# Kernel tuning notes

Hardware: AMD Instinct MI355X
Metric: run time of the kernel (lower is better)

## Reference

```python
import jax, jax.numpy as jnp
import numpy as np
from jax import lax

ROUTINGS = 3  # num_routing iterations


def _squash(v):
    # v: [..., num_atoms]
    norm = jnp.linalg.norm(v, axis=-1, keepdims=True)
    norm_sq = norm * norm
    return v / norm * (norm_sq / (1.0 + norm_sq))


def setup_inputs() -> dict:
    key = jax.random.key(0)
    k1, k2 = jax.random.split(key)
    B, H, Wd, Ci, Ai = 16, 32, 32, 8, 32
    k, Co, Ao = 5, 16, 16
    x = jax.random.normal(k1, (B, H, Wd, Ci, Ai), dtype=jnp.float32)
    # he_normal init for conv kernel [k, k, Ai, Co*Ao]
    fan_in = k * k * Ai
    W = jax.random.normal(k2, (k, k, Ai, Co * Ao), dtype=jnp.float32) * np.sqrt(2.0 / fan_in).astype(np.float32)
    b = jnp.full((1, 1, Co, Ao), 0.1, dtype=jnp.float32)  # constant(0.1) init
    return {"x": x, "W": W, "b": b}


def reference(x, W, b):
    B, H, Wd, Ci, Ai = x.shape
    k = W.shape[0]
    Co_Ao = W.shape[3]
    Co, Ao = b.shape[2], b.shape[3]
    # fold input capsules into the batch, conv over atoms
    xr = jnp.transpose(x, (0, 3, 1, 2, 4)).reshape(B * Ci, H, Wd, Ai)
    conv = lax.conv_general_dilated(
        xr, W, window_strides=(1, 1), padding="SAME",
        dimension_numbers=("NHWC", "HWIO", "NHWC"))  # [B*Ci, H, W, Co*Ao]
    Ho, Wo = conv.shape[1], conv.shape[2]
    votes = conv.reshape(B, Ci, Ho, Wo, Co, Ao)
    # biases broadcast over spatial dims: [1,1,Co,Ao] -> [Ho,Wo,Co,Ao]
    biases = jnp.broadcast_to(b, (Ho, Wo, Co, Ao))
    # dynamic routing (softmax variant): logits init to 0
    logits = jnp.zeros((B, Ci, Ho, Wo, Co), dtype=votes.dtype)
    activation = None
    for _ in range(ROUTINGS):
        route = jax.nn.softmax(logits, axis=-1)           # [B,Ci,Ho,Wo,Co]
        preact = jnp.sum(route[..., None] * votes, axis=1) + biases  # [B,Ho,Wo,Co,Ao]
        activation = _squash(preact)
        # agreement: sum over atoms of votes * activation
        logits = logits + jnp.sum(votes * activation[:, None], axis=-1)
    return activation
```

## Files before the change

### kernel.cpp

```cpp
#include <hip/hip_runtime.h>
#include <hip/hip_fp16.h>
#include <math.h>


typedef _Float16 f16;
typedef __attribute__((ext_vector_type(2))) _Float16 f16x2;
typedef __attribute__((ext_vector_type(8))) _Float16 f16x8;
typedef __attribute__((ext_vector_type(4))) float f32x4;

#define STRIDE_CI 1944
#define XB_OFF 0
#define WT_OFF 9437184

#define VIDX(p, cp, ao, co) ((((((p)*4 + (cp))*16 + (ao))*18) + (co)) + ((p) & 1))

static __device__ __forceinline__ float2 up16(unsigned int u) {
    union { unsigned int u; f16 h[2]; } c; c.u = u;
    return make_float2((float)c.h[0], (float)c.h[1]);
}

static __device__ __forceinline__ float fdot2u(unsigned int a, unsigned int b, float c) {
#if __has_builtin(__builtin_amdgcn_fdot2)
    union { unsigned int u; f16x2 h; } ua, ub;
    ua.u = a; ub.u = b;
    return __builtin_amdgcn_fdot2(ua.h, ub.h, c, false);
#else
    const float2 fa = up16(a), fb = up16(b);
    return c + fa.x * fb.x + fa.y * fb.y;
#endif
}

__global__ void prep(const float* __restrict__ x, const float* __restrict__ W,
                     f16* __restrict__ xb, f16* __restrict__ Wt) {
    __shared__ f16 lw[32 * 260];
    const int tid = threadIdx.x;
    const int bid = blockIdx.x;
    if (bid < 4608) {
        const int e4 = (bid * 256 + tid) * 4;
        const int c = e4 & 255;
        const int pix = e4 >> 8;
        const int wp = pix % 36;
        const int t = pix / 36;
        const int h = t & 31;
        const int b = t >> 5;
        const int w = wp - 2;
        f16 o[4] = {(f16)0.f, (f16)0.f, (f16)0.f, (f16)0.f};
        if ((unsigned)w < 32u) {
            const float4 v = *(const float4*)&x[(((b * 32 + h) * 32 + w) * 256) + c];
            o[0] = (f16)v.x; o[1] = (f16)v.y; o[2] = (f16)v.z; o[3] = (f16)v.w;
        }
        *(unsigned long long*)&xb[e4] = *(unsigned long long*)o;
    } else {
        const int k5 = bid - 4608;
        for (int rep = 0; rep < 32; ++rep) {
            const int idx = rep * 256 + tid;
            const int ai = idx >> 8, cc = idx & 255;
            lw[ai * 260 + cc] = (f16)W[(k5 * 32 + ai) * 256 + cc];
        }
        __syncthreads();
        for (int rep = 0; rep < 32; ++rep) {
            const int o = rep * 256 + tid;
            const int cc = o >> 5, ai = o & 31;
            Wt[k5 * 8192 + o] = lw[ai * 260 + cc];
        }
    }
}

__global__ __launch_bounds__(256, 3)
void caps_v6(const f16* __restrict__ xb, const f16* __restrict__ Wt,
             const float* __restrict__ bptr, float* __restrict__ out) {
    __shared__ __align__(16) unsigned char smraw[36864];
    f16* patch = (f16*)smraw;
    unsigned int* vl = (unsigned int*)smraw;
    __shared__ __align__(16) unsigned int route_l[8 * 16 * 4];
    __shared__ float logit_l[8 * 8 * 17];
    __shared__ float act_l[8 * 16 * 17];
    __shared__ float bias_l[256];

    const int tid = threadIdx.x;
    const int lane = tid & 63;
    const int wv = tid >> 6;
    const int bid = blockIdx.x;
    const int w0 = (bid & 3) * 8;
    const int h = (bid >> 2) & 31;
    const int b = bid >> 7;

    bias_l[tid] = bptr[tid];

    for (int e = tid; e < 1920; e += 256) {
        const int pos = e >> 5;
        const int ci = (e >> 2) & 7;
        const int s = e & 3;
        const int dh = pos / 12, dw = pos - dh * 12;
        const int gh = h + dh - 2;
        f16x8 v = {};
        if ((unsigned)gh < 32u)
            v = *(const f16x8*)&xb[(((b * 32 + gh) * 36) + (w0 + dw)) * 256 + ci * 32 + s * 8];
        *(f16x8*)&patch[ci * STRIDE_CI + pos * 32 + s * 8] = v;
    }
    __syncthreads();

    const int g = lane >> 4;
    const int q = lane & 15;
    const f16* aptr = patch + (lane & 7) * STRIDE_CI + ((lane >> 3) & 1) * 32 + g * 8;
    const f16* bbase = Wt + (wv * 64 + q) * 32 + g * 8;

    f32x4 acc[4][4];
#pragma unroll
    for (int rb = 0; rb < 4; ++rb)
#pragma unroll
        for (int ct = 0; ct < 4; ++ct) acc[rb][ct] = (f32x4)0.f;

    f16x8 Bc[4], Bn[4];
#pragma unroll
    for (int ct = 0; ct < 4; ++ct) {
        Bc[ct] = *(const f16x8*)(bbase + ct * 512);
        Bn[ct] = *(const f16x8*)(bbase + 8192 + ct * 512);
    }

    int k5 = 0;
#pragma unroll
    for (int kh = 0; kh < 5; ++kh) {
#pragma unroll
        for (int kw = 0; kw < 5; ++kw) {
            f16x8 Bf[4];
            if (k5 < 23) {
                const f16* bf = bbase + (k5 + 2) * 8192;
#pragma unroll
                for (int ct = 0; ct < 4; ++ct)
                    Bf[ct] = *(const f16x8*)(bf + ct * 512);
            }
            const f16* ap = aptr + (kh * 12 + kw) * 32;
            f16x8 A[4];
#pragma unroll
            for (int rb = 0; rb < 4; ++rb)
                A[rb] = *(const f16x8*)(ap + rb * 64);
#pragma unroll
            for (int rb = 0; rb < 4; ++rb)
#pragma unroll
                for (int ct = 0; ct < 4; ++ct)
                    acc[rb][ct] = __builtin_amdgcn_mfma_f32_16x16x32_f16(
                        A[rb], Bc[ct], acc[rb][ct], 0, 0, 0);
#pragma unroll
            for (int ct = 0; ct < 4; ++ct) { Bc[ct] = Bn[ct]; Bn[ct] = Bf[ct]; }
            ++k5;
        }
    }
    __syncthreads();

#pragma unroll
    for (int rb = 0; rb < 4; ++rb) {
        const int p = rb * 2 + (g >> 1);
        const int cpb = (g & 1) * 2;
#pragma unroll
        for (int ct = 0; ct < 4; ++ct) {
            const int co = wv * 4 + ct;
            union { f16 h[2]; unsigned int u; } c0, c1;
            c0.h[0] = (f16)acc[rb][ct].x; c0.h[1] = (f16)acc[rb][ct].y;
            c1.h[0] = (f16)acc[rb][ct].z; c1.h[1] = (f16)acc[rb][ct].w;
            vl[VIDX(p, cpb, q, co)] = c0.u;
            vl[VIDX(p, cpb + 1, q, co)] = c1.u;
        }
    }
    __syncthreads();

    const int rp = tid >> 5;
    const int coh = (tid >> 4) & 1;
    const int ao = tid & 15;
    const int pa = tid >> 5, cpa = (tid >> 3) & 3, co8 = tid & 7;
    const int swz = (pa & 1) * 4 + cpa;

    for (int it = 0; it < 3; ++it) {
        if (it > 0) {
            for (int i = tid; i < 1024; i += 256) {
                const int pp = i >> 7, ci = (i >> 4) & 7, co = i & 15;
                float lg = logit_l[(pp * 8 + ci) * 17 + co];
                float mx = lg;
#pragma unroll
                for (int m = 1; m < 16; m <<= 1) mx = fmaxf(mx, __shfl_xor(mx, m));
                float e = __expf(lg - mx);
                float s = e;
#pragma unroll
                for (int m = 1; m < 16; m <<= 1) s += __shfl_xor(s, m);
                const float r = e * __builtin_amdgcn_rcpf(s);
                const float rother = __shfl_xor(r, 16);
                if (((tid >> 4) & 1) == 0) {
                    union { f16 h[2]; unsigned int u; } pk;
                    pk.h[0] = (f16)r; pk.h[1] = (f16)rother;
                    route_l[(pp * 16 + co) * 4 + (ci >> 1)] = pk.u;
                }
            }
            __syncthreads();
        }

        float actv[8];
#pragma unroll
        for (int c8 = 0; c8 < 8; ++c8) {
            const int co = coh * 8 + c8;
            float pr = bias_l[co * 16 + ao];
            uint4 r4;
            if (it == 0) {
                r4.x = r4.y = r4.z = r4.w = 0x2C002C00u;
            } else {
                r4 = *(const uint4*)&route_l[(rp * 16 + co) * 4];
            }
            pr = fdot2u(vl[VIDX(rp, 0, ao, co)], r4.x, pr);
            pr = fdot2u(vl[VIDX(rp, 1, ao, co)], r4.y, pr);
            pr = fdot2u(vl[VIDX(rp, 2, ao, co)], r4.z, pr);
            pr = fdot2u(vl[VIDX(rp, 3, ao, co)], r4.w, pr);
            float sq = pr * pr;
#pragma unroll
            for (int m = 1; m < 16; m <<= 1) sq += __shfl_xor(sq, m);
            const float nrm = __builtin_amdgcn_sqrtf(sq);
            actv[c8] = pr * nrm * __builtin_amdgcn_rcpf(1.f + sq);
        }
#pragma unroll
        for (int c8 = 0; c8 < 8; ++c8)
            act_l[(rp * 16 + coh * 8 + c8) * 17 + ao] = actv[c8];
        __syncthreads();

        if (it < 2) {
            float d00 = 0.f, d01 = 0.f, d10 = 0.f, d11 = 0.f;
#pragma unroll
            for (int a0 = 0; a0 < 16; ++a0) {
                const int a = a0 ^ swz;
                const unsigned int wA = vl[VIDX(pa, cpa, a, co8)];
                const unsigned int wB = vl[VIDX(pa, cpa, a, co8 + 8)];
                const float aA = act_l[(pa * 16 + co8) * 17 + a];
                const float aB = act_l[(pa * 16 + co8 + 8) * 17 + a];
                const float2 fA = up16(wA), fB = up16(wB);
                d00 += fA.x * aA; d01 += fA.y * aA;
                d10 += fB.x * aB; d11 += fB.y * aB;
            }
            float* l0 = &logit_l[(pa * 8 + cpa * 2) * 17 + co8];
            if (it == 0) { l0[0] = d00; l0[17] = d01; l0[8] = d10; l0[25] = d11; }
            else         { l0[0] += d00; l0[17] += d01; l0[8] += d10; l0[25] += d11; }
            __syncthreads();
        }
    }

    const size_t base = ((size_t)((b * 32 + h) * 32 + w0)) * 256;
    for (int i = tid; i < 2048; i += 256) {
        const int pp = i >> 8, co = (i >> 4) & 15, aoo = i & 15;
        out[base + i] = act_l[(pp * 16 + co) * 17 + aoo];
    }
}

extern "C" void kernel_launch(void* const* d_in, const int* in_sizes, int n_in,
                              void* d_out, int out_size, void* d_ws, size_t ws_size,
                              hipStream_t stream) {
    const float* x  = (const float*)d_in[0];
    const float* W  = (const float*)d_in[1];
    const float* bb = (const float*)d_in[2];
    float* out = (float*)d_out;
    f16* xb = (f16*)((char*)d_ws + XB_OFF);
    f16* Wt = (f16*)((char*)d_ws + WT_OFF);

    hipLaunchKernelGGL(prep, dim3(4608 + 25), dim3(256), 0, stream, x, W, xb, Wt);
    hipLaunchKernelGGL(caps_v6, dim3(2048), dim3(256), 0, stream, xb, Wt, bb, out);
}
```

Measured before the change: 156.3 us.

## Prefetch A fragments and remap routing threads to drop act_l round-trips

```diff
diff --git a/kernel.cpp b/kernel.cpp
--- a/kernel.cpp
+++ b/kernel.cpp
@@ -67,14 +67,13 @@
 }
 
 __global__ __launch_bounds__(256, 3)
-void caps_v6(const f16* __restrict__ xb, const f16* __restrict__ Wt,
+void caps_v7(const f16* __restrict__ xb, const f16* __restrict__ Wt,
              const float* __restrict__ bptr, float* __restrict__ out) {
     __shared__ __align__(16) unsigned char smraw[36864];
     f16* patch = (f16*)smraw;
     unsigned int* vl = (unsigned int*)smraw;
-    __shared__ __align__(16) unsigned int route_l[8 * 16 * 4];
+    __shared__ __align__(16) uint4 route_l[8 * 16];
     __shared__ float logit_l[8 * 8 * 17];
-    __shared__ float act_l[8 * 16 * 17];
     __shared__ float bias_l[256];
 
     const int tid = threadIdx.x;
@@ -112,17 +111,28 @@
         for (int ct = 0; ct < 4; ++ct) acc[rb][ct] = (f32x4)0.f;
 
     f16x8 Bc[4], Bn[4];
+    f16x8 Ac[4], An[4];
 #pragma unroll
     for (int ct = 0; ct < 4; ++ct) {
         Bc[ct] = *(const f16x8*)(bbase + ct * 512);
         Bn[ct] = *(const f16x8*)(bbase + 8192 + ct * 512);
     }
+#pragma unroll
+    for (int rb = 0; rb < 4; ++rb)
+        Ac[rb] = *(const f16x8*)(aptr + rb * 64);
 
     int k5 = 0;
 #pragma unroll
     for (int kh = 0; kh < 5; ++kh) {
 #pragma unroll
         for (int kw = 0; kw < 5; ++kw) {
+            if (k5 < 24) {
+                const int n = k5 + 1;
+                const f16* apn = aptr + ((n / 5) * 12 + (n % 5)) * 32;
+#pragma unroll
+                for (int rb = 0; rb < 4; ++rb)
+                    An[rb] = *(const f16x8*)(apn + rb * 64);
+            }
             f16x8 Bf[4];
             if (k5 < 23) {
                 const f16* bf = bbase + (k5 + 2) * 8192;
@@ -130,17 +140,14 @@
                 for (int ct = 0; ct < 4; ++ct)
                     Bf[ct] = *(const f16x8*)(bf + ct * 512);
             }
-            const f16* ap = aptr + (kh * 12 + kw) * 32;
-            f16x8 A[4];
-#pragma unroll
-            for (int rb = 0; rb < 4; ++rb)
-                A[rb] = *(const f16x8*)(ap + rb * 64);
 #pragma unroll
             for (int rb = 0; rb < 4; ++rb)
 #pragma unroll
                 for (int ct = 0; ct < 4; ++ct)
                     acc[rb][ct] = __builtin_amdgcn_mfma_f32_16x16x32_f16(
-                        A[rb], Bc[ct], acc[rb][ct], 0, 0, 0);
+                        Ac[rb], Bc[ct], acc[rb][ct], 0, 0, 0);
+#pragma unroll
+            for (int rb = 0; rb < 4; ++rb) Ac[rb] = An[rb];
 #pragma unroll
             for (int ct = 0; ct < 4; ++ct) { Bc[ct] = Bn[ct]; Bn[ct] = Bf[ct]; }
             ++k5;
@@ -164,11 +171,10 @@
     }
     __syncthreads();
 
-    const int rp = tid >> 5;
-    const int coh = (tid >> 4) & 1;
-    const int ao = tid & 15;
-    const int pa = tid >> 5, cpa = (tid >> 3) & 3, co8 = tid & 7;
-    const int swz = (pa & 1) * 4 + cpa;
+    const int rp  = tid >> 5;
+    const int rco = (tid >> 1) & 15;
+    const int aoh = tid & 1;
+    unsigned int* route_d = (unsigned int*)route_l;
 
     for (int it = 0; it < 3; ++it) {
         if (it > 0) {
@@ -187,62 +193,68 @@
                 if (((tid >> 4) & 1) == 0) {
                     union { f16 h[2]; unsigned int u; } pk;
                     pk.h[0] = (f16)r; pk.h[1] = (f16)rother;
-                    route_l[(pp * 16 + co) * 4 + (ci >> 1)] = pk.u;
+                    route_d[(pp * 16 + co) * 4 + (ci >> 1)] = pk.u;
                 }
             }
             __syncthreads();
         }
 
+        uint4 r4;
+        if (it == 0) {
+            r4.x = r4.y = r4.z = r4.w = 0x2C002C00u;
+        } else {
+            r4 = route_l[rp * 16 + rco];
+        }
+        float pr[8];
+#pragma unroll
+        for (int a8 = 0; a8 < 8; ++a8) {
+            const int ao = aoh * 8 + a8;
+            float v = bias_l[rco * 16 + ao];
+            v = fdot2u(vl[VIDX(rp, 0, ao, rco)], r4.x, v);
+            v = fdot2u(vl[VIDX(rp, 1, ao, rco)], r4.y, v);
+            v = fdot2u(vl[VIDX(rp, 2, ao, rco)], r4.z, v);
+            v = fdot2u(vl[VIDX(rp, 3, ao, rco)], r4.w, v);
+            pr[a8] = v;
+        }
+        float sq = 0.f;
+#pragma unroll
+        for (int a8 = 0; a8 < 8; ++a8) sq += pr[a8] * pr[a8];
+        sq += __shfl_xor(sq, 1);
+        const float scale = __builtin_amdgcn_sqrtf(sq) * __builtin_amdgcn_rcpf(1.f + sq);
         float actv[8];
 #pragma unroll
-        for (int c8 = 0; c8 < 8; ++c8) {
-            const int co = coh * 8 + c8;
-            float pr = bias_l[co * 16 + ao];
-            uint4 r4;
-            if (it == 0) {
-                r4.x = r4.y = r4.z = r4.w = 0x2C002C00u;
-            } else {
-                r4 = *(const uint4*)&route_l[(rp * 16 + co) * 4];
-            }
-            pr = fdot2u(vl[VIDX(rp, 0, ao, co)], r4.x, pr);
-            pr = fdot2u(vl[VIDX(rp, 1, ao, co)], r4.y, pr);
-            pr = fdot2u(vl[VIDX(rp, 2, ao, co)], r4.z, pr);
-            pr = fdot2u(vl[VIDX(rp, 3, ao, co)], r4.w, pr);
-            float sq = pr * pr;
-#pragma unroll
-            for (int m = 1; m < 16; m <<= 1) sq += __shfl_xor(sq, m);
-            const float nrm = __builtin_amdgcn_sqrtf(sq);
-            actv[c8] = pr * nrm * __builtin_amdgcn_rcpf(1.f + sq);
-        }
-#pragma unroll
-        for (int c8 = 0; c8 < 8; ++c8)
-            act_l[(rp * 16 + coh * 8 + c8) * 17 + ao] = actv[c8];
-        __syncthreads();
+        for (int a8 = 0; a8 < 8; ++a8) actv[a8] = pr[a8] * scale;
 
         if (it < 2) {
-            float d00 = 0.f, d01 = 0.f, d10 = 0.f, d11 = 0.f;
-#pragma unroll
-            for (int a0 = 0; a0 < 16; ++a0) {
-                const int a = a0 ^ swz;
-                const unsigned int wA = vl[VIDX(pa, cpa, a, co8)];
-                const unsigned int wB = vl[VIDX(pa, cpa, a, co8 + 8)];
-                const float aA = act_l[(pa * 16 + co8) * 17 + a];
-                const float aB = act_l[(pa * 16 + co8 + 8) * 17 + a];
-                const float2 fA = up16(wA), fB = up16(wB);
-                d00 += fA.x * aA; d01 += fA.y * aA;
-                d10 += fB.x * aB; d11 += fB.y * aB;
-            }
-            float* l0 = &logit_l[(pa * 8 + cpa * 2) * 17 + co8];
-            if (it == 0) { l0[0] = d00; l0[17] = d01; l0[8] = d10; l0[25] = d11; }
-            else         { l0[0] += d00; l0[17] += d01; l0[8] += d10; l0[25] += d11; }
+            float part[8];
+#pragma unroll
+            for (int cp = 0; cp < 4; ++cp) {
+                float e = 0.f, o = 0.f;
+#pragma unroll
+                for (int a8 = 0; a8 < 8; ++a8) {
+                    const float2 f = up16(vl[VIDX(rp, cp, aoh * 8 + a8, rco)]);
+                    e += f.x * actv[a8];
+                    o += f.y * actv[a8];
+                }
+                part[cp * 2] = e; part[cp * 2 + 1] = o;
+            }
+#pragma unroll
+            for (int ci = 0; ci < 8; ++ci) part[ci] += __shfl_xor(part[ci], 1);
+            if (aoh == 0) {
+#pragma unroll
+                for (int ci = 0; ci < 8; ++ci) {
+                    float* lp = &logit_l[(rp * 8 + ci) * 17 + rco];
+                    if (it == 0) *lp = part[ci];
+                    else         *lp += part[ci];
+                }
+            }
             __syncthreads();
-        }
-    }
-
-    const size_t base = ((size_t)((b * 32 + h) * 32 + w0)) * 256;
-    for (int i = tid; i < 2048; i += 256) {
-        const int pp = i >> 8, co = (i >> 4) & 15, aoo = i & 15;
-        out[base + i] = act_l[(pp * 16 + co) * 17 + aoo];
+        } else {
+            const size_t base = ((size_t)((b * 32 + h) * 32 + w0)) * 256;
+            float* dst = out + base + rp * 256 + rco * 16 + aoh * 8;
+            *(float4*)dst       = make_float4(actv[0], actv[1], actv[2], actv[3]);
+            *(float4*)(dst + 4) = make_float4(actv[4], actv[5], actv[6], actv[7]);
+        }
     }
 }
 
@@ -257,5 +269,5 @@
     f16* Wt = (f16*)((char*)d_ws + WT_OFF);
 
     hipLaunchKernelGGL(prep, dim3(4608 + 25), dim3(256), 0, stream, x, W, xb, Wt);
-    hipLaunchKernelGGL(caps_v6, dim3(2048), dim3(256), 0, stream, xb, Wt, bb, out);
-}
+    hipLaunchKernelGGL(caps_v7, dim3(2048), dim3(256), 0, stream, xb, Wt, bb, out);
+}
```

After: 147.4 us. 1.06x faster.
